# Performance work log

Measured on AMD Instinct MI355X. Metric: run time of the kernel, lower is better.

Reference implementation:

```python
import jax, jax.numpy as jnp
import numpy as np

H = 8          # num_heads
EPS = 1e-6     # layernorm epsilon
NEG_INF = -1e9


def _ln(x, g, b):
    m = jnp.mean(x, axis=-1, keepdims=True)
    v = jnp.mean(jnp.square(x - m), axis=-1, keepdims=True)
    return g * (x - m) * jax.lax.rsqrt(v + EPS) + b


def _mha(xq, kv, wq, wk, wv, wo, bias):
    # xq: [B,Tq,D], kv: [B,Tk,D]; weights [D,D]. Returns (out [B,Tq,D], weights [B,H,Tq,Tk]).
    B, Tq, D = xq.shape
    dh = D // H
    q = (xq @ wq) * (dh ** -0.5)
    k = kv @ wk
    v = kv @ wv
    q = q.reshape(B, Tq, H, dh).transpose(0, 2, 1, 3)
    k = k.reshape(B, -1, H, dh).transpose(0, 2, 1, 3)
    v = v.reshape(B, -1, H, dh).transpose(0, 2, 1, 3)
    logits = jnp.einsum('bhqd,bhkd->bhqk', q, k)
    if bias is not None:
        logits = logits + bias
    w = jax.nn.softmax(logits, axis=-1)
    out = jnp.einsum('bhqk,bhkd->bhqd', w, v).transpose(0, 2, 1, 3).reshape(B, Tq, D)
    return out @ wo, w


def setup_inputs() -> dict:
    key = jax.random.key(0)
    ks = jax.random.split(key, 16)
    B, Td, Te, D, F, L = 2, 2048, 2048, 512, 2048, 2
    s = 0.02
    inp = {
        'x': jax.random.normal(ks[0], (B, Td, D), jnp.float32),
        'enc_a': jax.random.normal(ks[1], (B, Te, D), jnp.float32),
        'enc_c': jax.random.normal(ks[2], (B, Te, D), jnp.float32),
        'sa_wq': jax.random.normal(ks[3], (L, D, D), jnp.float32) * s,
        'sa_wk': jax.random.normal(ks[4], (L, D, D), jnp.float32) * s,
        'sa_wv': jax.random.normal(ks[5], (L, D, D), jnp.float32) * s,
        'sa_wo': jax.random.normal(ks[6], (L, D, D), jnp.float32) * s,
        'ed_wq': jax.random.normal(ks[7], (L, D, D), jnp.float32) * s,
        'ed_wk': jax.random.normal(ks[8], (L, D, D), jnp.float32) * s,
        'ed_wv': jax.random.normal(ks[9], (L, D, D), jnp.float32) * s,
        'ed_wo': jax.random.normal(ks[10], (L, D, D), jnp.float32) * s,
        'ffn_w1': jax.random.normal(ks[11], (L, D, F), jnp.float32) * s,
        'ffn_w2': jax.random.normal(ks[12], (L, F, D), jnp.float32) * s,
        'ln1_g': jnp.ones((L, D), jnp.float32), 'ln1_b': jnp.zeros((L, D), jnp.float32),
        'ln2_g': jnp.ones((L, D), jnp.float32), 'ln2_b': jnp.zeros((L, D), jnp.float32),
        'ln3_g': jnp.ones((L, D), jnp.float32), 'ln3_b': jnp.zeros((L, D), jnp.float32),
        'out_g': jnp.ones((D,), jnp.float32), 'out_b': jnp.zeros((D,), jnp.float32),
    }
    return inp


def reference(x, enc_a, enc_c, sa_wq, sa_wk, sa_wv, sa_wo, ed_wq, ed_wk, ed_wv, ed_wo,
              ffn_w1, ffn_w2, ln1_g, ln1_b, ln2_g, ln2_b, ln3_g, ln3_b, out_g, out_b):
    B, T, D = x.shape
    L = sa_wq.shape[0]
    # decoder self-attention causal bias, broadcast over [B,H]
    causal = jnp.where(jnp.tril(jnp.ones((T, T), bool)), 0.0, NEG_INF)[None, None]
    avg = None
    for i in range(L):
        h = _ln(x, ln1_g[i], ln1_b[i])
        y, _ = _mha(h, h, sa_wq[i], sa_wk[i], sa_wv[i], sa_wo[i], causal)
        x = x + y  # residual (dropout inactive at eval)
        h = _ln(x, ln2_g[i], ln2_b[i])
        y0, _ = _mha(h, enc_a, ed_wq[i], ed_wk[i], ed_wv[i], ed_wo[i], None)
        y1, w = _mha(h, enc_c, ed_wq[i], ed_wk[i], ed_wv[i], ed_wo[i], None)
        # original overwrites attn_scores with second call's head-averaged weights
        scores = jnp.mean(w, axis=1) / L
        avg = scores if avg is None else avg + scores
        x = x + y0 + y1
        h = _ln(x, ln3_g[i], ln3_b[i])
        x = x + jax.nn.relu(h @ ffn_w1[i]) @ ffn_w2[i]
    x = _ln(x, out_g, out_b)
    return x, avg
```

## Files before the change

kernel.cpp:

```cpp
#include <hip/hip_runtime.h>
#include <hip/hip_bf16.h>

#define BB 2
#define TT 2048
#define DD 512
#define FF 2048
#define HH 8
#define DH 64
#define LL 2
#define MM (BB*TT)

typedef __attribute__((ext_vector_type(8))) short bf16x8;
typedef __attribute__((ext_vector_type(4))) float f32x4;

__device__ __forceinline__ float bf2f(unsigned short u) {
    return __uint_as_float(((unsigned int)u) << 16);
}
__device__ __forceinline__ unsigned short f2bf(float f) {
    unsigned int u = __float_as_uint(f);
    u += 0x7fffu + ((u >> 16) & 1u);
    return (unsigned short)(u >> 16);
}
__device__ __forceinline__ unsigned int cvtpk(float a, float b) {
    unsigned int r;
    asm("v_cvt_pk_bf16_f32 %0, %1, %2" : "=v"(r) : "v"(a), "v"(b));
    return r;
}
__device__ __forceinline__ void gload16(const void* g, void* l) {
    __builtin_amdgcn_global_load_lds((__attribute__((address_space(1))) void*)g,
                                     (__attribute__((address_space(3))) void*)l, 16, 0, 0);
}

template<bool BF16OUT>
__global__ __launch_bounds__(256) void ln_kernel(const float* __restrict__ x,
                                                 const float* __restrict__ g,
                                                 const float* __restrict__ b,
                                                 void* __restrict__ out)
{
    const int row = blockIdx.x;
    const int tid = threadIdx.x;
    const float2 v = ((const float2*)(x + (size_t)row * DD))[tid];
    float s = v.x + v.y;
    float q = v.x * v.x + v.y * v.y;
    #pragma unroll
    for (int off = 32; off; off >>= 1) {
        s += __shfl_down(s, off);
        q += __shfl_down(q, off);
    }
    __shared__ float ss[4], qq[4];
    const int wid = tid >> 6;
    if ((tid & 63) == 0) { ss[wid] = s; qq[wid] = q; }
    __syncthreads();
    s = ss[0] + ss[1] + ss[2] + ss[3];
    q = qq[0] + qq[1] + qq[2] + qq[3];
    const float mean = s * (1.0f / DD);
    const float var = q * (1.0f / DD) - mean * mean;
    const float inv = rsqrtf(var + 1e-6f);
    const float2 gg = ((const float2*)g)[tid];
    const float2 bb = ((const float2*)b)[tid];
    const float ox = gg.x * (v.x - mean) * inv + bb.x;
    const float oy = gg.y * (v.y - mean) * inv + bb.y;
    if (BF16OUT) {
        const unsigned int pk = cvtpk(ox, oy);
        ((unsigned int*)((unsigned short*)out + (size_t)row * DD))[tid] = pk;
    } else {
        float2 o; o.x = ox; o.y = oy;
        ((float2*)((float*)out + (size_t)row * DD))[tid] = o;
    }
}

struct CvtEJob { const float* s; unsigned short* d; };
struct CvtEJobs2 { CvtEJob j[2]; };

__global__ __launch_bounds__(256) void cvt_kernel(CvtEJobs2 P, int n)
{
    const CvtEJob jb = P.j[blockIdx.z];
    const int i = (blockIdx.x * 256 + threadIdx.x) * 8;
    if (i >= n) return;
    const float4 a = *(const float4*)(jb.s + i);
    const float4 b = *(const float4*)(jb.s + i + 4);
    unsigned int o[4];
    o[0] = cvtpk(a.x, a.y); o[1] = cvtpk(a.z, a.w);
    o[2] = cvtpk(b.x, b.y); o[3] = cvtpk(b.z, b.w);
    *(bf16x8*)(jb.d + i) = *(bf16x8*)o;
}

struct CvtTJob { const float* s; unsigned short* d; int K; int N; };
struct CvtTJobs20 { CvtTJob j[20]; };

__global__ __launch_bounds__(256) void cvtT_kernel(CvtTJobs20 P)
{
    __shared__ float t[32][33];
    const CvtTJob jb = P.j[blockIdx.z];
    const int gk = blockIdx.y << 5, gn = blockIdx.x << 5;
    if (gk >= jb.K || gn >= jb.N) return;
    const int tx = threadIdx.x & 31, ty = threadIdx.x >> 5;
    #pragma unroll
    for (int i = 0; i < 4; ++i)
        t[ty + i * 8][tx] = jb.s[(size_t)(gk + ty + i * 8) * jb.N + gn + tx];
    __syncthreads();
    #pragma unroll
    for (int i = 0; i < 4; ++i)
        jb.d[(size_t)(gn + ty + i * 8) * jb.K + gk + tx] = f2bf(t[tx][ty + i * 8]);
}

struct GemmJob {
    const unsigned short* A;
    const unsigned short* Wt;
    const float* res;
    float* Cf;
    unsigned short* Cb;
    unsigned short* Ct;
    float scale;
    int relu;
};
struct GemmJobs6 { GemmJob j[6]; };

__global__ __launch_bounds__(256, 2) void gemm_mfma(GemmJobs6 P, int M, int N, int K)
{
    __shared__ __align__(16) unsigned char lds[32768];
    const GemmJob jb = P.j[blockIdx.z];
    const int tid = threadIdx.x, lane = tid & 63, w = tid >> 6;
    const int bn = blockIdx.x << 7, bm = blockIdx.y << 7;
    const int wr = (w >> 1) << 6, wc = (w & 1) << 6;
    const size_t strA = (size_t)K * 2;

    f32x4 acc[4][4] = {};
    const int akey = (lane & 7) << 4;
    const int frow = lane & 15;
    const int kq = (lane >> 4) << 4;

    for (int kt = 0; kt < K; kt += 64) {
        __syncthreads();
        #pragma unroll
        for (int c = 0; c < 4; ++c) {
            const int q = c * 4 + w;
            const int o = (q << 10) + (lane << 4);
            const int row = o >> 7;
            const int colb = (o & 127) ^ ((row & 7) << 4);
            gload16((const char*)jb.A + (size_t)(bm + row) * strA + kt * 2 + colb,
                    lds + (q << 10));
            gload16((const char*)jb.Wt + (size_t)(bn + row) * strA + kt * 2 + colb,
                    lds + 16384 + (q << 10));
        }
        asm volatile("s_waitcnt vmcnt(0)" ::: "memory");
        __syncthreads();
        #pragma unroll
        for (int kk = 0; kk < 2; ++kk) {
            bf16x8 av[4], bv[4];
            #pragma unroll
            for (int i = 0; i < 4; ++i) {
                const int rA = wr + (i << 4) + frow;
                av[i] = *(const bf16x8*)(lds + (rA << 7) + ((((kk << 6) + kq)) ^ akey));
                const int rB = wc + (i << 4) + frow;
                bv[i] = *(const bf16x8*)(lds + 16384 + (rB << 7) + ((((kk << 6) + kq)) ^ akey));
            }
            #pragma unroll
            for (int i = 0; i < 4; ++i)
                #pragma unroll
                for (int j = 0; j < 4; ++j)
                    acc[i][j] = __builtin_amdgcn_mfma_f32_16x16x32_bf16(av[i], bv[j], acc[i][j], 0, 0, 0);
        }
    }

    const int crow0 = (lane >> 4) << 2;
    const int ccol = lane & 15;
    if (jb.Ct) {
        #pragma unroll
        for (int i = 0; i < 4; ++i)
            #pragma unroll
            for (int j = 0; j < 4; ++j) {
                const int gm = bm + wr + (i << 4) + crow0;
                const int gn = bn + wc + (j << 4) + ccol;
                const int bI = gm >> 11, t = gm & 2047;
                const int hI = gn >> 6, d = gn & 63;
                uint2 pk;
                pk.x = cvtpk(acc[i][j][0], acc[i][j][1]);
                pk.y = cvtpk(acc[i][j][2], acc[i][j][3]);
                *(uint2*)(jb.Ct + ((size_t)((bI * HH + hI) * DH + d)) * TT + t) = pk;
            }
        return;
    }
    #pragma unroll
    for (int i = 0; i < 4; ++i) {
        #pragma unroll
        for (int j = 0; j < 4; ++j) {
            #pragma unroll
            for (int r = 0; r < 4; ++r) {
                const int gm = bm + wr + (i << 4) + crow0 + r;
                const int gn = bn + wc + (j << 4) + ccol;
                float v = acc[i][j][r] * jb.scale;
                if (jb.relu) v = fmaxf(v, 0.f);
                const size_t idx = (size_t)gm * N + gn;
                if (jb.res) v += jb.res[idx];
                if (jb.Cf) jb.Cf[idx] = v;
                if (jb.Cb) jb.Cb[idx] = f2bf(v);
            }
        }
    }
}

template<bool CAUSAL, bool DUAL, int NQ>
__global__ __launch_bounds__(256, (NQ == 1) ? 4 : 3) void flash_mfma(
    const unsigned short* __restrict__ q,
    const unsigned short* __restrict__ ka, const unsigned short* __restrict__ vta,
    const unsigned short* __restrict__ kc, const unsigned short* __restrict__ vtc,
    unsigned short* __restrict__ Opart,
    float* __restrict__ mlpart)
{
    __shared__ __align__(16) char lds[(NQ == 1) ? 40960 : 49152];
    const int tid = threadIdx.x;
    const int lane = tid & 63, w = tid >> 6;
    const int g4 = lane >> 4, c = lane & 15;

    constexpr int GX = (32 / NQ) * 2;
    const int f = blockIdx.x + GX * (blockIdx.y + 8 * blockIdx.z);
    const int xcd = f & 7;
    const int tt = f >> 3;
    const int u = tt % GX;
    const int half = u & 1, jq = u >> 1;
    const int grp = (tt / GX) * 8 + xcd;
    int b, h, which;
    if (DUAL) { which = grp & 1; b = (grp >> 1) & 1; h = grp >> 2; }
    else      { which = 0;       b = grp & 1;        h = grp >> 1; }
    const int q0 = jq * (64 * NQ);
    const int q0w = q0 + w * (16 * NQ);
    const int kendw = q0w + 16 * NQ;

    const unsigned short* k  = (DUAL && which) ? kc : ka;
    const unsigned short* vt = (DUAL && which) ? vtc : vta;
    const int slot = (DUAL ? (which << 1) : 0) + half;
    unsigned short* Od = Opart + (size_t)slot * MM * DD;
    float* mld = mlpart + (size_t)slot * (BB * HH * TT * 2);

    bf16x8 Qf[NQ][2];
    #pragma unroll
    for (int jb = 0; jb < NQ; ++jb) {
        const unsigned short* qp = q + (size_t)(b * TT + q0w + (jb << 4) + c) * DD + h * DH + (g4 << 3);
        Qf[jb][0] = *(const bf16x8*)qp;
        Qf[jb][1] = *(const bf16x8*)(qp + 32);
    }
    const char* kbase = (const char*)(k + (size_t)b * TT * DD + h * DH);
    const char* vtb   = (const char*)(vt + (size_t)(b * HH + h) * DH * TT);
    char* Pw = lds + 32768 + w * (NQ * 2048);
    const int pkey = (c & 7) << 4;

    f32x4 O[NQ][4] = {};
    float mval[NQ], lpart[NQ];
    #pragma unroll
    for (int jb = 0; jb < NQ; ++jb) { mval[jb] = -1e30f; lpart[jb] = 0.f; }

    const int ntt = CAUSAL ? ((q0 + 64 * NQ) >> 6) : (TT >> 6);
    const int tBeg = half ? ((ntt + 1) >> 1) : 0;
    const int tEnd = half ? ntt : ((ntt + 1) >> 1);

    auto STAGE = [&](int t, int sel) {
        const int kt = t << 6;
        char* Kb = lds + sel * 8192;
        char* Vb = lds + 16384 + sel * 8192;
        #pragma unroll
        for (int c8 = 0; c8 < 2; ++c8) {
            const int qc = (c8 << 2) + w;
            const int o = (qc << 10) + (lane << 4);
            const int row = o >> 7;
            const int colb = (o & 127) ^ ((row & 7) << 4);
            gload16(kbase + (size_t)(kt + row) * (DD * 2) + colb, Kb + (qc << 10));
            gload16(vtb + (size_t)row * (TT * 2) + kt * 2 + colb, Vb + (qc << 10));
        }
    };

    if (tBeg < tEnd) {
        STAGE(tBeg, 0);
        asm volatile("s_waitcnt vmcnt(0)" ::: "memory");
        __syncthreads();

        for (int t = tBeg; t < tEnd; ++t) {
            const int cur = (t - tBeg) & 1;
            if (t + 1 < tEnd) STAGE(t + 1, cur ^ 1);
            const int kt = t << 6;

            if (!CAUSAL || kt < kendw) {
                const char* Kb = lds + cur * 8192;
                const char* Vb = lds + 16384 + cur * 8192;

                f32x4 s[NQ][4] = {};
                #pragma unroll
                for (int kk = 0; kk < 2; ++kk) {
                    bf16x8 av[4];
                    #pragma unroll
                    for (int i = 0; i < 4; ++i) {
                        const int r = (i << 4) + c;
                        av[i] = *(const bf16x8*)(Kb + (r << 7) + (((kk << 6) + (g4 << 4)) ^ ((r & 7) << 4)));
                    }
                    #pragma unroll
                    for (int i = 0; i < 4; ++i)
                        #pragma unroll
                        for (int jb = 0; jb < NQ; ++jb)
                            s[jb][i] = __builtin_amdgcn_mfma_f32_16x16x32_bf16(av[i], Qf[jb][kk], s[jb][i], 0, 0, 0);
                }

                #pragma unroll
                for (int jb = 0; jb < NQ; ++jb) {
                    const int qbase = q0w + (jb << 4);
                    if (CAUSAL && kt + 63 > qbase) {
                        #pragma unroll
                        for (int i = 0; i < 4; ++i)
                            #pragma unroll
                            for (int r = 0; r < 4; ++r)
                                if (kt + (i << 4) + (g4 << 2) + r > qbase + c) s[jb][i][r] = -1e30f;
                    }
                    float pmax = -1e30f;
                    #pragma unroll
                    for (int i = 0; i < 4; ++i)
                        #pragma unroll
                        for (int r = 0; r < 4; ++r) pmax = fmaxf(pmax, s[jb][i][r]);
                    if (__any(pmax > mval[jb] + 11.f)) {
                        float mx = fmaxf(pmax, __shfl_xor(pmax, 16));
                        mx = fmaxf(mx, __shfl_xor(mx, 32));
                        const float mn = fmaxf(mval[jb], mx);
                        const float scf = exp2f(mval[jb] - mn);
                        lpart[jb] *= scf;
                        #pragma unroll
                        for (int r = 0; r < 4; ++r) {
                            const float fr = __shfl(scf, (g4 << 2) + r);
                            #pragma unroll
                            for (int jj = 0; jj < 4; ++jj) O[jb][jj][r] *= fr;
                        }
                        mval[jb] = mn;
                    }
                    float ps = 0.f;
                    #pragma unroll
                    for (int i = 0; i < 4; ++i)
                        #pragma unroll
                        for (int r = 0; r < 4; ++r) {
                            const float p = exp2f(s[jb][i][r] - mval[jb]);
                            s[jb][i][r] = p;
                            ps += p;
                        }
                    lpart[jb] += ps;
                    #pragma unroll
                    for (int i = 0; i < 4; ++i) {
                        uint2 pk;
                        pk.x = cvtpk(s[jb][i][0], s[jb][i][1]);
                        pk.y = cvtpk(s[jb][i][2], s[jb][i][3]);
                        const int baddr = (((jb << 4) + c) << 7) + (((i << 4) + (g4 << 2)) << 1);
                        *(uint2*)(Pw + (baddr ^ pkey)) = pk;
                    }
                }
                asm volatile("s_waitcnt lgkmcnt(0)" ::: "memory");
                __builtin_amdgcn_sched_barrier(0);

                #pragma unroll
                for (int kk = 0; kk < 2; ++kk) {
                    bf16x8 pa[NQ];
                    #pragma unroll
                    for (int jb = 0; jb < NQ; ++jb)
                        pa[jb] = *(const bf16x8*)(Pw + (((((jb << 4) + c) << 7) + (kk << 6) + (g4 << 4)) ^ pkey));
                    #pragma unroll
                    for (int jj = 0; jj < 4; ++jj) {
                        const int d = (jj << 4) + c;
                        const bf16x8 vb = *(const bf16x8*)(Vb + (d << 7) + (((kk << 6) + (g4 << 4)) ^ ((d & 7) << 4)));
                        #pragma unroll
                        for (int jb = 0; jb < NQ; ++jb)
                            O[jb][jj] = __builtin_amdgcn_mfma_f32_16x16x32_bf16(pa[jb], vb, O[jb][jj], 0, 0, 0);
                    }
                }
            }

            asm volatile("s_waitcnt vmcnt(0)" ::: "memory");
            __syncthreads();
        }
    }

    #pragma unroll
    for (int jb = 0; jb < NQ; ++jb) {
        float l2 = lpart[jb] + __shfl_xor(lpart[jb], 16);
        const float ltot = l2 + __shfl_xor(l2, 32);
        #pragma unroll
        for (int jj = 0; jj < 4; ++jj)
            #pragma unroll
            for (int r = 0; r < 4; ++r) {
                const int qr = q0w + (jb << 4) + (g4 << 2) + r;
                Od[(size_t)(b * TT + qr) * DD + h * DH + (jj << 4) + c] = f2bf(O[jb][jj][r]);
            }
        if (lane < 16) {
            const size_t mi = (((size_t)b * HH + h) * TT + q0w + (jb << 4) + lane) * 2;
            mld[mi] = mval[jb];
            mld[mi + 1] = ltot;
        }
    }
}

template<int NS, bool STOREML>
__global__ __launch_bounds__(256) void merge_kernel(
    const unsigned short* __restrict__ Opart, const float* __restrict__ mlpart,
    unsigned short* __restrict__ out, float* __restrict__ ml_out)
{
    const int row = blockIdx.x;
    const int b = row >> 11, rt = row & 2047;
    const int t = threadIdx.x;
    const int d0 = t << 1, h = d0 >> 6;
    float acc0 = 0.f, acc1 = 0.f;
    float Ms = 0.f, Ls = 0.f;
    #pragma unroll
    for (int s = 0; s < NS; ++s) {
        const size_t mb = ((size_t)(b * HH + h) * TT + rt) * 2;
        const float* mp0 = mlpart + (size_t)(s * 2 + 0) * (BB * HH * TT * 2) + mb;
        const float* mp1 = mlpart + (size_t)(s * 2 + 1) * (BB * HH * TT * 2) + mb;
        const float m0 = mp0[0], l0 = mp0[1], m1 = mp1[0], l1 = mp1[1];
        const float M = fmaxf(m0, m1);
        const float a0 = exp2f(m0 - M), a1 = exp2f(m1 - M);
        const float inv = 1.f / (a0 * l0 + a1 * l1);
        const unsigned short* p0 = Opart + (size_t)(s * 2 + 0) * MM * DD + (size_t)row * DD + d0;
        const unsigned short* p1 = Opart + (size_t)(s * 2 + 1) * MM * DD + (size_t)row * DD + d0;
        acc0 += (a0 * bf2f(p0[0]) + a1 * bf2f(p1[0])) * inv;
        acc1 += (a0 * bf2f(p0[1]) + a1 * bf2f(p1[1])) * inv;
        if (STOREML && s == NS - 1) { Ms = M; Ls = a0 * l0 + a1 * l1; }
    }
    ((unsigned int*)(out + (size_t)row * DD))[t] = cvtpk(acc0, acc1);
    if (STOREML && (d0 & 63) == 0) {
        float* mo = ml_out + ((size_t)(b * HH + h) * TT + rt) * 2;
        mo[0] = Ms; mo[1] = Ls;
    }
}

__global__ __launch_bounds__(64) void avg_mfma_kernel(const unsigned short* __restrict__ qm,
                                                      const unsigned short* __restrict__ kcm,
                                                      const float* __restrict__ ml,
                                                      float* __restrict__ avg, int first)
{
    __shared__ __align__(16) unsigned char ldsQ[8192];
    __shared__ __align__(16) unsigned char ldsK[8192];
    __shared__ float sM[8][64];
    __shared__ float sIL[8][64];
    const int lane = threadIdx.x;
    const int kt0 = blockIdx.x << 6, q0 = blockIdx.y << 6, b = blockIdx.z;

    #pragma unroll
    for (int h = 0; h < 8; ++h) {
        const float* mp = ml + (((size_t)(b * HH + h) * TT) + q0 + lane) * 2;
        sM[h][lane] = mp[0];
        sIL[h][lane] = 1.f / mp[1];
    }

    float avac[4][4][4] = {};
    const int akey = (lane & 7) << 4;
    const int frow = lane & 15;
    const int kq = (lane >> 4) << 4;
    const int crow0 = (lane >> 4) << 2;

    for (int h = 0; h < 8; ++h) {
        __syncthreads();
        #pragma unroll
        for (int c = 0; c < 8; ++c) {
            const int o = (c << 10) + (lane << 4);
            const int row = o >> 7;
            const int colb = (o & 127) ^ ((row & 7) << 4);
            gload16((const char*)qm + ((size_t)(b * TT + q0 + row) * DD + h * DH) * 2 + colb,
                    ldsQ + (c << 10));
            gload16((const char*)kcm + ((size_t)(b * TT + kt0 + row) * DD + h * DH) * 2 + colb,
                    ldsK + (c << 10));
        }
        asm volatile("s_waitcnt vmcnt(0)" ::: "memory");
        __syncthreads();
        f32x4 s[4][4] = {};
        #pragma unroll
        for (int kk = 0; kk < 2; ++kk) {
            bf16x8 qv[4], kv[4];
            #pragma unroll
            for (int i = 0; i < 4; ++i) {
                qv[i] = *(const bf16x8*)(ldsQ + (((i << 4) + frow) << 7) + (((kk << 6) + kq) ^ akey));
                kv[i] = *(const bf16x8*)(ldsK + (((i << 4) + frow) << 7) + (((kk << 6) + kq) ^ akey));
            }
            #pragma unroll
            for (int i = 0; i < 4; ++i)
                #pragma unroll
                for (int j = 0; j < 4; ++j)
                    s[i][j] = __builtin_amdgcn_mfma_f32_16x16x32_bf16(qv[i], kv[j], s[i][j], 0, 0, 0);
        }
        #pragma unroll
        for (int i = 0; i < 4; ++i)
            #pragma unroll
            for (int j = 0; j < 4; ++j)
                #pragma unroll
                for (int r = 0; r < 4; ++r) {
                    const int qr = (i << 4) + crow0 + r;
                    avac[i][j][r] += exp2f(s[i][j][r] - sM[h][qr]) * sIL[h][qr];
                }
    }

    float* dst = avg + ((size_t)b * TT + q0) * TT + kt0;
    #pragma unroll
    for (int i = 0; i < 4; ++i)
        #pragma unroll
        for (int j = 0; j < 4; ++j)
            #pragma unroll
            for (int r = 0; r < 4; ++r) {
                const int qr = (i << 4) + crow0 + r;
                const int kc = (j << 4) + (lane & 15);
                const float v = avac[i][j][r] * (1.f / (HH * LL));
                float* p = dst + (size_t)qr * TT + kc;
                *p = first ? v : (*p + v);
            }
}

extern "C" void kernel_launch(void* const* d_in, const int* in_sizes, int n_in,
                              void* d_out, int out_size, void* d_ws, size_t ws_size,
                              hipStream_t stream)
{
    const float* x_in   = (const float*)d_in[0];
    const float* enc_a  = (const float*)d_in[1];
    const float* enc_c  = (const float*)d_in[2];
    const float* sa_wq0 = (const float*)d_in[3];
    const float* sa_wk0 = (const float*)d_in[4];
    const float* sa_wv0 = (const float*)d_in[5];
    const float* sa_wo0 = (const float*)d_in[6];
    const float* ed_wq0 = (const float*)d_in[7];
    const float* ed_wk0 = (const float*)d_in[8];
    const float* ed_wv0 = (const float*)d_in[9];
    const float* ed_wo0 = (const float*)d_in[10];
    const float* ffn_w10 = (const float*)d_in[11];
    const float* ffn_w20 = (const float*)d_in[12];
    const float* ln1_g0 = (const float*)d_in[13];
    const float* ln1_b0 = (const float*)d_in[14];
    const float* ln2_g0 = (const float*)d_in[15];
    const float* ln2_b0 = (const float*)d_in[16];
    const float* ln3_g0 = (const float*)d_in[17];
    const float* ln3_b0 = (const float*)d_in[18];
    const float* out_g  = (const float*)d_in[19];
    const float* out_b  = (const float*)d_in[20];

    const size_t NTD = (size_t)MM * DD;
    const size_t MB = 1u << 20;
    char* W = (char*)d_ws;
    float*          x_buf   = (float*)(W);
    unsigned short* h_bf    = (unsigned short*)(W + 8 * MB);
    unsigned short* q_bf    = (unsigned short*)(W + 12 * MB);
    unsigned short* k1_bf   = (unsigned short*)(W + 16 * MB);
    unsigned short* vt1     = (unsigned short*)(W + 20 * MB);
    unsigned short* k2_bf   = (unsigned short*)(W + 24 * MB);
    unsigned short* vt2     = (unsigned short*)(W + 28 * MB);
    unsigned short* attnA   = (unsigned short*)(W + 32 * MB);
    unsigned short* attnS   = (unsigned short*)(W + 36 * MB);
    float*          ml_buf  = (float*)(W + 40 * MB);
    unsigned short* encA_bf = (unsigned short*)(W + 41 * MB);
    unsigned short* encC_bf = (unsigned short*)(W + 45 * MB);
    unsigned short* wbf     = (unsigned short*)(W + 49 * MB);
    unsigned short* Opart   = (unsigned short*)(W + 68 * MB);
    float*          mlpart  = (float*)(W + 84 * MB);
    unsigned short* ffn_bf  = q_bf;

    unsigned short* w1t = wbf + (size_t)16 * DD * DD;
    unsigned short* w2t = w1t + (size_t)2 * DD * FF;
    auto wd = [&](int l, int which) { return wbf + ((size_t)(l * 8 + which)) * DD * DD; };

    float* x_out   = (float*)d_out;
    float* avg_out = (float*)d_out + NTD;

    hipMemcpyAsync(x_buf, x_in, NTD * sizeof(float), hipMemcpyDeviceToDevice, stream);

    {
        CvtTJobs20 J{};
        const float* srcs[8] = {sa_wq0, sa_wk0, sa_wv0, sa_wo0, ed_wq0, ed_wk0, ed_wv0, ed_wo0};
        for (int l = 0; l < LL; ++l)
            for (int t = 0; t < 8; ++t)
                J.j[l * 8 + t] = {srcs[t] + (size_t)l * DD * DD, wd(l, t), DD, DD};
        for (int l = 0; l < LL; ++l) {
            J.j[16 + l] = {ffn_w10 + (size_t)l * DD * FF, w1t + (size_t)l * FF * DD, DD, FF};
            J.j[18 + l] = {ffn_w20 + (size_t)l * FF * DD, w2t + (size_t)l * DD * FF, FF, DD};
        }
        cvtT_kernel<<<dim3(FF / 32, FF / 32, 20), 256, 0, stream>>>(J);
    }
    {
        CvtEJobs2 J{};
        J.j[0] = {enc_a, encA_bf};
        J.j[1] = {enc_c, encC_bf};
        cvt_kernel<<<dim3(NTD / 8 / 256, 1, 2), 256, 0, stream>>>(J, (int)NTD);
    }

    const dim3 flashSelfG(64, HH, BB);
    const dim3 flashCrossG(32, HH, BB * 2);
    const dim3 avgG(TT / 64, TT / 64, BB);
    const float qscale = 0.125f * 1.4426950408889634f;

    for (int i = 0; i < LL; ++i) {
        const size_t fOff = (size_t)i * DD * FF;
        const size_t lOff = (size_t)i * DD;

        ln_kernel<true><<<MM, 256, 0, stream>>>(x_buf, ln1_g0 + lOff, ln1_b0 + lOff, h_bf);
        {
            GemmJobs6 J{};
            J.j[0] = {h_bf, wd(i, 0), nullptr, nullptr, q_bf, nullptr, qscale, 0};
            J.j[1] = {h_bf, wd(i, 1), nullptr, nullptr, k1_bf, nullptr, 1.f, 0};
            J.j[2] = {h_bf, wd(i, 2), nullptr, nullptr, nullptr, vt1, 1.f, 0};
            gemm_mfma<<<dim3(DD / 128, MM / 128, 3), 256, 0, stream>>>(J, MM, DD, DD);
        }
        flash_mfma<true, false, 1><<<flashSelfG, 256, 0, stream>>>(
            q_bf, k1_bf, vt1, nullptr, nullptr, Opart, mlpart);
        merge_kernel<1, false><<<MM, 256, 0, stream>>>(Opart, mlpart, attnA, nullptr);
        {
            GemmJobs6 J{};
            J.j[0] = {attnA, wd(i, 3), x_buf, x_buf, nullptr, nullptr, 1.f, 0};
            gemm_mfma<<<dim3(DD / 128, MM / 128, 1), 256, 0, stream>>>(J, MM, DD, DD);
        }

        ln_kernel<true><<<MM, 256, 0, stream>>>(x_buf, ln2_g0 + lOff, ln2_b0 + lOff, h_bf);
        {
            GemmJobs6 J{};
            J.j[0] = {h_bf,    wd(i, 4), nullptr, nullptr, q_bf, nullptr, qscale, 0};
            J.j[1] = {encA_bf, wd(i, 5), nullptr, nullptr, k1_bf, nullptr, 1.f, 0};
            J.j[2] = {encA_bf, wd(i, 6), nullptr, nullptr, nullptr, vt1, 1.f, 0};
            J.j[3] = {encC_bf, wd(i, 5), nullptr, nullptr, k2_bf, nullptr, 1.f, 0};
            J.j[4] = {encC_bf, wd(i, 6), nullptr, nullptr, nullptr, vt2, 1.f, 0};
            gemm_mfma<<<dim3(DD / 128, MM / 128, 5), 256, 0, stream>>>(J, MM, DD, DD);
        }
        flash_mfma<false, true, 2><<<flashCrossG, 256, 0, stream>>>(
            q_bf, k1_bf, vt1, k2_bf, vt2, Opart, mlpart);
        merge_kernel<2, true><<<MM, 256, 0, stream>>>(Opart, mlpart, attnS, ml_buf);
        avg_mfma_kernel<<<avgG, 64, 0, stream>>>(q_bf, k2_bf, ml_buf, avg_out, (i == 0) ? 1 : 0);
        {
            GemmJobs6 J{};
            J.j[0] = {attnS, wd(i, 7), x_buf, x_buf, nullptr, nullptr, 1.f, 0};
            gemm_mfma<<<dim3(DD / 128, MM / 128, 1), 256, 0, stream>>>(J, MM, DD, DD);
        }

        ln_kernel<true><<<MM, 256, 0, stream>>>(x_buf, ln3_g0 + lOff, ln3_b0 + lOff, h_bf);
        {
            GemmJobs6 J{};
            J.j[0] = {h_bf, w1t + fOff, nullptr, nullptr, ffn_bf, nullptr, 1.f, 1};
            gemm_mfma<<<dim3(FF / 128, MM / 128, 1), 256, 0, stream>>>(J, MM, FF, DD);
        }
        {
            GemmJobs6 J{};
            J.j[0] = {ffn_bf, w2t + fOff, x_buf, x_buf, nullptr, nullptr, 1.f, 0};
            gemm_mfma<<<dim3(DD / 128, MM / 128, 1), 256, 0, stream>>>(J, MM, DD, FF);
        }
    }

    ln_kernel<false><<<MM, 256, 0, stream>>>(x_buf, out_g, out_b, x_out);
}
```

Baseline: 644.8 us.

## Batch cross-attn K/V projections into self-attn GEMM and restructure avg kernel

When the workspace is large enough, the encoder K/V projections for the cross-attention are moved into the same batched GEMM launch as the self-attention QKV, writing into separate buffers. This leaves only the Q projection in the second launch and gives the first launch more blocks to fill the GPU. The avg-weights kernel now uses 256 threads with double-buffered LDS staging, so the next head's loads overlap with compute. It recomputes the merged m/l statistics directly from mlpart, which drops the merge kernel's ml output, and writes its results as float4 stores. The cost is extra workspace, and the fused path only runs when the workspace is at least 97 MB.

```diff
diff --git a/kernel.cpp b/kernel.cpp
--- a/kernel.cpp
+++ b/kernel.cpp
@@ -114,9 +114,9 @@
     float scale;
     int relu;
 };
-struct GemmJobs6 { GemmJob j[6]; };
-
-__global__ __launch_bounds__(256, 2) void gemm_mfma(GemmJobs6 P, int M, int N, int K)
+struct GemmJobs8 { GemmJob j[8]; };
+
+__global__ __launch_bounds__(256, 2) void gemm_mfma(GemmJobs8 P, int M, int N, int K)
 {
     __shared__ __align__(16) unsigned char lds[32768];
     const GemmJob jb = P.j[blockIdx.z];
@@ -391,17 +391,16 @@
     }
 }
 
-template<int NS, bool STOREML>
+template<int NS>
 __global__ __launch_bounds__(256) void merge_kernel(
     const unsigned short* __restrict__ Opart, const float* __restrict__ mlpart,
-    unsigned short* __restrict__ out, float* __restrict__ ml_out)
+    unsigned short* __restrict__ out)
 {
     const int row = blockIdx.x;
     const int b = row >> 11, rt = row & 2047;
     const int t = threadIdx.x;
     const int d0 = t << 1, h = d0 >> 6;
     float acc0 = 0.f, acc1 = 0.f;
-    float Ms = 0.f, Ls = 0.f;
     #pragma unroll
     for (int s = 0; s < NS; ++s) {
         const size_t mb = ((size_t)(b * HH + h) * TT + rt) * 2;
@@ -415,93 +414,97 @@
         const unsigned short* p1 = Opart + (size_t)(s * 2 + 1) * MM * DD + (size_t)row * DD + d0;
         acc0 += (a0 * bf2f(p0[0]) + a1 * bf2f(p1[0])) * inv;
         acc1 += (a0 * bf2f(p0[1]) + a1 * bf2f(p1[1])) * inv;
-        if (STOREML && s == NS - 1) { Ms = M; Ls = a0 * l0 + a1 * l1; }
     }
     ((unsigned int*)(out + (size_t)row * DD))[t] = cvtpk(acc0, acc1);
-    if (STOREML && (d0 & 63) == 0) {
-        float* mo = ml_out + ((size_t)(b * HH + h) * TT + rt) * 2;
-        mo[0] = Ms; mo[1] = Ls;
-    }
-}
-
-__global__ __launch_bounds__(64) void avg_mfma_kernel(const unsigned short* __restrict__ qm,
-                                                      const unsigned short* __restrict__ kcm,
-                                                      const float* __restrict__ ml,
-                                                      float* __restrict__ avg, int first)
-{
-    __shared__ __align__(16) unsigned char ldsQ[8192];
-    __shared__ __align__(16) unsigned char ldsK[8192];
-    __shared__ float sM[8][64];
-    __shared__ float sIL[8][64];
-    const int lane = threadIdx.x;
+}
+
+__global__ __launch_bounds__(256) void avg_mfma_kernel(const unsigned short* __restrict__ qm,
+                                                       const unsigned short* __restrict__ kcm,
+                                                       const float* __restrict__ mlpart,
+                                                       float* __restrict__ avg, int first)
+{
+    __shared__ __align__(16) unsigned char ldsQ[2][8192];
+    __shared__ __align__(16) unsigned char ldsK[2][8192];
+    const int tid = threadIdx.x;
+    const int lane = tid & 63, w = tid >> 6;
+    const int g4 = lane >> 4, c = lane & 15;
     const int kt0 = blockIdx.x << 6, q0 = blockIdx.y << 6, b = blockIdx.z;
-
+    const int qrow = q0 + (w << 4) + c;
+
+    float m8[8], il8[8];
     #pragma unroll
     for (int h = 0; h < 8; ++h) {
-        const float* mp = ml + (((size_t)(b * HH + h) * TT) + q0 + lane) * 2;
-        sM[h][lane] = mp[0];
-        sIL[h][lane] = 1.f / mp[1];
-    }
-
-    float avac[4][4][4] = {};
-    const int akey = (lane & 7) << 4;
-    const int frow = lane & 15;
-    const int kq = (lane >> 4) << 4;
-    const int crow0 = (lane >> 4) << 2;
-
-    for (int h = 0; h < 8; ++h) {
-        __syncthreads();
-        #pragma unroll
-        for (int c = 0; c < 8; ++c) {
-            const int o = (c << 10) + (lane << 4);
+        const size_t mb = ((size_t)(b * HH + h) * TT + qrow) * 2;
+        const float* mp2 = mlpart + (size_t)2 * (BB * HH * TT * 2) + mb;
+        const float* mp3 = mlpart + (size_t)3 * (BB * HH * TT * 2) + mb;
+        const float m2 = mp2[0], l2v = mp2[1], m3 = mp3[0], l3v = mp3[1];
+        const float M = fmaxf(m2, m3);
+        const float L = exp2f(m2 - M) * l2v + exp2f(m3 - M) * l3v;
+        m8[h] = M;
+        il8[h] = 1.f / L;
+    }
+
+    auto STAGE = [&](int h, int sel) {
+        #pragma unroll
+        for (int u2 = 0; u2 < 2; ++u2) {
+            const int qc = (u2 << 2) + w;
+            const int o = (qc << 10) + (lane << 4);
             const int row = o >> 7;
             const int colb = (o & 127) ^ ((row & 7) << 4);
             gload16((const char*)qm + ((size_t)(b * TT + q0 + row) * DD + h * DH) * 2 + colb,
-                    ldsQ + (c << 10));
+                    &ldsQ[sel][qc << 10]);
             gload16((const char*)kcm + ((size_t)(b * TT + kt0 + row) * DD + h * DH) * 2 + colb,
-                    ldsK + (c << 10));
-        }
+                    &ldsK[sel][qc << 10]);
+        }
+    };
+
+    f32x4 avac[4] = {};
+    STAGE(0, 0);
+    asm volatile("s_waitcnt vmcnt(0)" ::: "memory");
+    __syncthreads();
+
+    for (int h = 0; h < 8; ++h) {
+        const int cur = h & 1;
+        if (h + 1 < 8) STAGE(h + 1, cur ^ 1);
+        f32x4 s[4] = {};
+        #pragma unroll
+        for (int kk = 0; kk < 2; ++kk) {
+            const int qrl = (w << 4) + c;
+            const bf16x8 qf = *(const bf16x8*)(&ldsQ[cur][(qrl << 7) + (((kk << 6) + (g4 << 4)) ^ ((qrl & 7) << 4))]);
+            #pragma unroll
+            for (int i = 0; i < 4; ++i) {
+                const int r = (i << 4) + c;
+                const bf16x8 av = *(const bf16x8*)(&ldsK[cur][(r << 7) + (((kk << 6) + (g4 << 4)) ^ ((r & 7) << 4))]);
+                s[i] = __builtin_amdgcn_mfma_f32_16x16x32_bf16(av, qf, s[i], 0, 0, 0);
+            }
+        }
+        #pragma unroll
+        for (int i = 0; i < 4; ++i)
+            #pragma unroll
+            for (int r = 0; r < 4; ++r)
+                avac[i][r] += exp2f(s[i][r] - m8[h]) * il8[h];
         asm volatile("s_waitcnt vmcnt(0)" ::: "memory");
         __syncthreads();
-        f32x4 s[4][4] = {};
-        #pragma unroll
-        for (int kk = 0; kk < 2; ++kk) {
-            bf16x8 qv[4], kv[4];
-            #pragma unroll
-            for (int i = 0; i < 4; ++i) {
-                qv[i] = *(const bf16x8*)(ldsQ + (((i << 4) + frow) << 7) + (((kk << 6) + kq) ^ akey));
-                kv[i] = *(const bf16x8*)(ldsK + (((i << 4) + frow) << 7) + (((kk << 6) + kq) ^ akey));
-            }
-            #pragma unroll
-            for (int i = 0; i < 4; ++i)
-                #pragma unroll
-                for (int j = 0; j < 4; ++j)
-                    s[i][j] = __builtin_amdgcn_mfma_f32_16x16x32_bf16(qv[i], kv[j], s[i][j], 0, 0, 0);
-        }
-        #pragma unroll
-        for (int i = 0; i < 4; ++i)
-            #pragma unroll
-            for (int j = 0; j < 4; ++j)
-                #pragma unroll
-                for (int r = 0; r < 4; ++r) {
-                    const int qr = (i << 4) + crow0 + r;
-                    avac[i][j][r] += exp2f(s[i][j][r] - sM[h][qr]) * sIL[h][qr];
-                }
-    }
-
-    float* dst = avg + ((size_t)b * TT + q0) * TT + kt0;
-    #pragma unroll
-    for (int i = 0; i < 4; ++i)
-        #pragma unroll
-        for (int j = 0; j < 4; ++j)
-            #pragma unroll
-            for (int r = 0; r < 4; ++r) {
-                const int qr = (i << 4) + crow0 + r;
-                const int kc = (j << 4) + (lane & 15);
-                const float v = avac[i][j][r] * (1.f / (HH * LL));
-                float* p = dst + (size_t)qr * TT + kc;
-                *p = first ? v : (*p + v);
-            }
+    }
+
+    float* dst = avg + (size_t)(b * TT + qrow) * TT + kt0;
+    #pragma unroll
+    for (int i = 0; i < 4; ++i) {
+        const int kc = (i << 4) + (g4 << 2);
+        float4 vv;
+        vv.x = avac[i][0] * (1.f / (HH * LL));
+        vv.y = avac[i][1] * (1.f / (HH * LL));
+        vv.z = avac[i][2] * (1.f / (HH * LL));
+        vv.w = avac[i][3] * (1.f / (HH * LL));
+        float4* p = (float4*)(dst + kc);
+        if (first) {
+            *p = vv;
+        } else {
+            float4 old = *p;
+            old.x += vv.x; old.y += vv.y; old.z += vv.z; old.w += vv.w;
+            *p = old;
+        }
+    }
 }
 
 extern "C" void kernel_launch(void* const* d_in, const int* in_sizes, int n_in,
@@ -542,13 +545,16 @@
     unsigned short* vt2     = (unsigned short*)(W + 28 * MB);
     unsigned short* attnA   = (unsigned short*)(W + 32 * MB);
     unsigned short* attnS   = (unsigned short*)(W + 36 * MB);
-    float*          ml_buf  = (float*)(W + 40 * MB);
     unsigned short* encA_bf = (unsigned short*)(W + 41 * MB);
     unsigned short* encC_bf = (unsigned short*)(W + 45 * MB);
     unsigned short* wbf     = (unsigned short*)(W + 49 * MB);
     unsigned short* Opart   = (unsigned short*)(W + 68 * MB);
     float*          mlpart  = (float*)(W + 84 * MB);
     unsigned short* ffn_bf  = q_bf;
+
+    const bool fused = (ws_size >= (size_t)97 * MB);
+    unsigned short* k1c  = fused ? (unsigned short*)(W + 88 * MB) : k1_bf;
+    unsigned short* vt1c = fused ? (unsigned short*)(W + 92 * MB) : vt1;
 
     unsigned short* w1t = wbf + (size_t)16 * DD * DD;
     unsigned short* w2t = w1t + (size_t)2 * DD * FF;
@@ -588,8 +594,18 @@
         const size_t lOff = (size_t)i * DD;
 
         ln_kernel<true><<<MM, 256, 0, stream>>>(x_buf, ln1_g0 + lOff, ln1_b0 + lOff, h_bf);
-        {
-            GemmJobs6 J{};
+        if (fused) {
+            GemmJobs8 J{};
+            J.j[0] = {h_bf,    wd(i, 0), nullptr, nullptr, q_bf, nullptr, qscale, 0};
+            J.j[1] = {h_bf,    wd(i, 1), nullptr, nullptr, k1_bf, nullptr, 1.f, 0};
+            J.j[2] = {h_bf,    wd(i, 2), nullptr, nullptr, nullptr, vt1, 1.f, 0};
+            J.j[3] = {encA_bf, wd(i, 5), nullptr, nullptr, k1c, nullptr, 1.f, 0};
+            J.j[4] = {encA_bf, wd(i, 6), nullptr, nullptr, nullptr, vt1c, 1.f, 0};
+            J.j[5] = {encC_bf, wd(i, 5), nullptr, nullptr, k2_bf, nullptr, 1.f, 0};
+            J.j[6] = {encC_bf, wd(i, 6), nullptr, nullptr, nullptr, vt2, 1.f, 0};
+            gemm_mfma<<<dim3(DD / 128, MM / 128, 7), 256, 0, stream>>>(J, MM, DD, DD);
+        } else {
+            GemmJobs8 J{};
             J.j[0] = {h_bf, wd(i, 0), nullptr, nullptr, q_bf, nullptr, qscale, 0};
             J.j[1] = {h_bf, wd(i, 1), nullptr, nullptr, k1_bf, nullptr, 1.f, 0};
             J.j[2] = {h_bf, wd(i, 2), nullptr, nullptr, nullptr, vt1, 1.f, 0};
@@ -597,16 +613,20 @@
         }
         flash_mfma<true, false, 1><<<flashSelfG, 256, 0, stream>>>(
             q_bf, k1_bf, vt1, nullptr, nullptr, Opart, mlpart);
-        merge_kernel<1, false><<<MM, 256, 0, stream>>>(Opart, mlpart, attnA, nullptr);
+        merge_kernel<1><<<MM, 256, 0, stream>>>(Opart, mlpart, attnA);
         {
-            GemmJobs6 J{};
+            GemmJobs8 J{};
             J.j[0] = {attnA, wd(i, 3), x_buf, x_buf, nullptr, nullptr, 1.f, 0};
             gemm_mfma<<<dim3(DD / 128, MM / 128, 1), 256, 0, stream>>>(J, MM, DD, DD);
         }
 
         ln_kernel<true><<<MM, 256, 0, stream>>>(x_buf, ln2_g0 + lOff, ln2_b0 + lOff, h_bf);
-        {
-            GemmJobs6 J{};
+        if (fused) {
+            GemmJobs8 J{};
+            J.j[0] = {h_bf, wd(i, 4), nullptr, nullptr, q_bf, nullptr, qscale, 0};
+            gemm_mfma<<<dim3(DD / 128, MM / 128, 1), 256, 0, stream>>>(J, MM, DD, DD);
+        } else {
+            GemmJobs8 J{};
             J.j[0] = {h_bf,    wd(i, 4), nullptr, nullptr, q_bf, nullptr, qscale, 0};
             J.j[1] = {encA_bf, wd(i, 5), nullptr, nullptr, k1_bf, nullptr, 1.f, 0};
             J.j[2] = {encA_bf, wd(i, 6), nullptr, nullptr, nullptr, vt1, 1.f, 0};
@@ -615,23 +635,23 @@
             gemm_mfma<<<dim3(DD / 128, MM / 128, 5), 256, 0, stream>>>(J, MM, DD, DD);
         }
         flash_mfma<false, true, 2><<<flashCrossG, 256, 0, stream>>>(
-            q_bf, k1_bf, vt1, k2_bf, vt2, Opart, mlpart);
-        merge_kernel<2, true><<<MM, 256, 0, stream>>>(Opart, mlpart, attnS, ml_buf);
-        avg_mfma_kernel<<<avgG, 64, 0, stream>>>(q_bf, k2_bf, ml_buf, avg_out, (i == 0) ? 1 : 0);
+            q_bf, k1c, vt1c, k2_bf, vt2, Opart, mlpart);
+        merge_kernel<2><<<MM, 256, 0, stream>>>(Opart, mlpart, attnS);
+        avg_mfma_kernel<<<avgG, 256, 0, stream>>>(q_bf, k2_bf, mlpart, avg_out, (i == 0) ? 1 : 0);
         {
-            GemmJobs6 J{};
+            GemmJobs8 J{};
             J.j[0] = {attnS, wd(i, 7), x_buf, x_buf, nullptr, nullptr, 1.f, 0};
             gemm_mfma<<<dim3(DD / 128, MM / 128, 1), 256, 0, stream>>>(J, MM, DD, DD);
         }
 
         ln_kernel<true><<<MM, 256, 0, stream>>>(x_buf, ln3_g0 + lOff, ln3_b0 + lOff, h_bf);
         {
-            GemmJobs6 J{};
+            GemmJobs8 J{};
             J.j[0] = {h_bf, w1t + fOff, nullptr, nullptr, ffn_bf, nullptr, 1.f, 1};
             gemm_mfma<<<dim3(FF / 128, MM / 128, 1), 256, 0, stream>>>(J, MM, FF, DD);
         }
         {
-            GemmJobs6 J{};
+            GemmJobs8 J{};
             J.j[0] = {ffn_bf, w2t + fOff, x_buf, x_buf, nullptr, nullptr, 1.f, 0};
             gemm_mfma<<<dim3(DD / 128, MM / 128, 1), 256, 0, stream>>>(J, MM, DD, FF);
         }
```

Measured after the change: 727.6 us. +12.8%, slower.
